# Kernel tuning notes

Measured on AMD Instinct MI355X. Metric: run time of the kernel, lower is better.

Reference implementation:

```python
import jax, jax.numpy as jnp
import numpy as np

OUT = 7          # output_size
SR = 2           # sampling_ratio
SCALES = (0.25, 0.125, 0.0625, 0.03125)
K_MIN, K_MAX = 2, 5   # -log2(scales[0]), -log2(scales[-1])
CANON_SCALE, CANON_LVL, EPS = 224.0, 4.0, 1e-6


def _roi_align_level(feat, b_idx, boxes, scale):
    """ROIAlign (maskrcnn-benchmark, non-aligned) of all boxes on one level.
    feat: [B,C,H,W], b_idx: [N] int, boxes: [N,4] xyxy in image coords.
    Returns [N,C,OUT,OUT]."""
    N = boxes.shape[0]
    H, W = feat.shape[2], feat.shape[3]
    x1 = boxes[:, 0] * scale
    y1 = boxes[:, 1] * scale
    x2 = boxes[:, 2] * scale
    y2 = boxes[:, 3] * scale
    roi_w = jnp.maximum(x2 - x1, 1.0)
    roi_h = jnp.maximum(y2 - y1, 1.0)
    bin_w = roi_w / OUT
    bin_h = roi_h / OUT
    # sample positions inside each bin, in bin units: [OUT*SR]
    sub = (jnp.arange(SR, dtype=feat.dtype) + 0.5) / SR
    grid1d = (jnp.arange(OUT, dtype=feat.dtype)[:, None] + sub[None, :]).reshape(-1)
    ys = y1[:, None] + bin_h[:, None] * grid1d[None, :]   # [N, OUT*SR]
    xs = x1[:, None] + bin_w[:, None] * grid1d[None, :]   # [N, OUT*SR]
    K = OUT * SR
    Yf = jnp.broadcast_to(ys[:, :, None], (N, K, K)).reshape(N, K * K)
    Xf = jnp.broadcast_to(xs[:, None, :], (N, K, K)).reshape(N, K * K)
    valid = (Yf >= -1.0) & (Yf <= H) & (Xf >= -1.0) & (Xf <= W)
    y = jnp.clip(Yf, 0.0, H - 1)
    x = jnp.clip(Xf, 0.0, W - 1)
    y0 = jnp.floor(y).astype(jnp.int32)
    x0 = jnp.floor(x).astype(jnp.int32)
    y1i = jnp.minimum(y0 + 1, H - 1)
    x1i = jnp.minimum(x0 + 1, W - 1)
    ly = y - y0
    lx = x - x0
    hy = 1.0 - ly
    hx = 1.0 - lx
    b = b_idx[:, None]  # [N,1] broadcasts with [N,K*K]
    def g(yi, xi):
        return feat[b, :, yi, xi]  # [N, K*K, C]
    val = (g(y0, x0) * (hy * hx)[..., None]
           + g(y0, x1i) * (hy * lx)[..., None]
           + g(y1i, x0) * (ly * hx)[..., None]
           + g(y1i, x1i) * (ly * lx)[..., None])
    val = jnp.where(valid[..., None], val, 0.0)
    # [N, OUT, SR, OUT, SR, C] -> average sampling points -> [N, OUT, OUT, C]
    val = val.reshape(N, OUT, SR, OUT, SR, -1).mean(axis=(2, 4))
    return jnp.transpose(val, (0, 3, 1, 2))  # [N, C, OUT, OUT]


def _map_levels(boxes):
    # BoxList.area with TO_REMOVE = 1 (xyxy mode)
    area = (boxes[:, 2] - boxes[:, 0] + 1.0) * (boxes[:, 3] - boxes[:, 1] + 1.0)
    s = jnp.sqrt(area)
    lvl = jnp.floor(CANON_LVL + jnp.log2(s / CANON_SCALE + EPS))
    lvl = jnp.clip(lvl, K_MIN, K_MAX)
    return lvl.astype(jnp.int32) - K_MIN  # 0..3


def setup_inputs() -> dict:
    key = jax.random.key(0)
    ks = jax.random.split(key, 10)
    N = 1024
    H_img, W_img = 800.0, 1216.0
    x1 = jax.random.uniform(ks[0], (N,), minval=0.0, maxval=W_img - 64.0)
    y1 = jax.random.uniform(ks[1], (N,), minval=0.0, maxval=H_img - 64.0)
    w = jax.random.uniform(ks[2], (N,), minval=8.0, maxval=500.0)
    h = jax.random.uniform(ks[3], (N,), minval=8.0, maxval=500.0)
    x2 = jnp.minimum(x1 + w, W_img - 1.0)
    y2 = jnp.minimum(y1 + h, H_img - 1.0)
    boxes = jnp.stack([x1, y1, x2, y2], axis=1).astype(jnp.float32)
    box_batch_idx = jnp.sort(jax.random.randint(ks[4], (N,), 0, 2)).astype(jnp.int32)
    f0 = jax.random.normal(ks[5], (2, 256, 200, 304), dtype=jnp.float32)
    f1 = jax.random.normal(ks[6], (2, 256, 100, 152), dtype=jnp.float32)
    f2 = jax.random.normal(ks[7], (2, 256, 50, 76), dtype=jnp.float32)
    f3 = jax.random.normal(ks[8], (2, 256, 25, 38), dtype=jnp.float32)
    return {"f0": f0, "f1": f1, "f2": f2, "f3": f3,
            "boxes": boxes, "box_batch_idx": box_batch_idx}


def reference(f0, f1, f2, f3, boxes, box_batch_idx):
    feats = (f0, f1, f2, f3)
    levels = _map_levels(boxes)  # [N] in 0..3
    out = None
    for lvl, (feat, scale) in enumerate(zip(feats, SCALES)):
        pooled = _roi_align_level(feat, box_batch_idx, boxes, scale)
        mask = (levels == lvl)[:, None, None, None]
        part = jnp.where(mask, pooled, 0.0)
        out = part if out is None else out + part
    return out  # [N, C, OUT, OUT]
```

## Files before the change

kernel.cpp:

```cpp
#include <hip/hip_runtime.h>
#include <math.h>

#define TILE_F 1792
#define B448   448
#define B896   896
#define NCH    8
#define MAXI   7
#define MAXIP  4
#define MAXI4  2
#define MAXK3  6

typedef __attribute__((address_space(3))) void lds_void;
typedef const __attribute__((address_space(1))) void g_void;

__device__ __forceinline__ void dma16(const float* g, float* l) {
  __builtin_amdgcn_global_load_lds((g_void*)g, (lds_void*)l, 16, 0, 0);
}
__device__ __forceinline__ void dma4(const float* g, float* l) {
  __builtin_amdgcn_global_load_lds((g_void*)g, (lds_void*)l, 4, 0, 0);
}
__device__ __forceinline__ void wait_vmcnt(int k) {
  switch (k) {
    case 0:  asm volatile("s_waitcnt vmcnt(0)"  ::: "memory"); break;
    case 1:  asm volatile("s_waitcnt vmcnt(1)"  ::: "memory"); break;
    case 2:  asm volatile("s_waitcnt vmcnt(2)"  ::: "memory"); break;
    case 3:  asm volatile("s_waitcnt vmcnt(3)"  ::: "memory"); break;
    case 4:  asm volatile("s_waitcnt vmcnt(4)"  ::: "memory"); break;
    case 5:  asm volatile("s_waitcnt vmcnt(5)"  ::: "memory"); break;
    case 6:  asm volatile("s_waitcnt vmcnt(6)"  ::: "memory"); break;
    case 7:  asm volatile("s_waitcnt vmcnt(7)"  ::: "memory"); break;
    case 8:  asm volatile("s_waitcnt vmcnt(8)"  ::: "memory"); break;
    case 9:  asm volatile("s_waitcnt vmcnt(9)"  ::: "memory"); break;
    case 10: asm volatile("s_waitcnt vmcnt(10)" ::: "memory"); break;
    case 11: asm volatile("s_waitcnt vmcnt(11)" ::: "memory"); break;
    case 12: asm volatile("s_waitcnt vmcnt(12)" ::: "memory"); break;
    case 13: asm volatile("s_waitcnt vmcnt(13)" ::: "memory"); break;
    case 14: asm volatile("s_waitcnt vmcnt(14)" ::: "memory"); break;
    case 15: asm volatile("s_waitcnt vmcnt(15)" ::: "memory"); break;
    case 16: asm volatile("s_waitcnt vmcnt(16)" ::: "memory"); break;
    case 17: asm volatile("s_waitcnt vmcnt(17)" ::: "memory"); break;
    default: asm volatile("s_waitcnt vmcnt(18)" ::: "memory"); break;
  }
}

#define COMPUTE_STORE(TP, CC)                                                  \
  if (lane < 49) {                                                             \
    float acc = 0.0f;                                                          \
    _Pragma("unroll")                                                          \
    for (int sy = 0; sy < 2; ++sy) {                                           \
      _Pragma("unroll")                                                        \
      for (int sx = 0; sx < 2; ++sx) {                                         \
        const float w00 = (TP)[rT[sy] + Cc0[sx]];                              \
        const float w01 = (TP)[rT[sy] + Cc1[sx]];                              \
        const float w10 = (TP)[rB[sy] + Cc0[sx]];                              \
        const float w11 = (TP)[rB[sy] + Cc1[sx]];                              \
        const float bil = HY[sy] * (HX[sx] * w00 + LX[sx] * w01)               \
                        + LY[sy] * (HX[sx] * w10 + LX[sx] * w11);              \
        acc += (VY[sy] * VX[sx]) * bil;                                        \
      }                                                                        \
    }                                                                          \
    outp[(CC) * 49] = acc * 0.25f;                                             \
  }

__global__ __launch_bounds__(128) void pooler_kernel(
    const float* __restrict__ f0, const float* __restrict__ f1,
    const float* __restrict__ f2, const float* __restrict__ f3,
    const float* __restrict__ boxes, const int* __restrict__ bidx,
    float* __restrict__ out, int N)
{
  __shared__ __align__(16) float tile[2][TILE_F];
  const int tid  = threadIdx.x;
  const int wave = tid >> 6, lane = tid & 63;
  const int n    = blockIdx.y;
  if (n >= N) return;

  const float bx1 = boxes[4*n+0], by1 = boxes[4*n+1];
  const float bx2 = boxes[4*n+2], by2 = boxes[4*n+3];
  const float area = (bx2 - bx1 + 1.0f) * (by2 - by1 + 1.0f);
  const float s    = sqrtf(area);
  int lvl = (int)floorf(4.0f + log2f(s / 224.0f + 1e-6f));
  lvl = lvl < 2 ? 2 : (lvl > 5 ? 5 : lvl);
  const int li = lvl - 2;

  int H, W; const float* feat; float scale;
  switch (li) {
    case 0:  feat = f0; H = 200; W = 304; scale = 0.25f;    break;
    case 1:  feat = f1; H = 100; W = 152; scale = 0.125f;   break;
    case 2:  feat = f2; H = 50;  W = 76;  scale = 0.0625f;  break;
    default: feat = f3; H = 25;  W = 38;  scale = 0.03125f; break;
  }
  const int b = bidx[n];
  const float x1s = bx1 * scale, y1s = by1 * scale;
  const float roiw = fmaxf(bx2 * scale - x1s, 1.0f);
  const float roih = fmaxf(by2 * scale - y1s, 1.0f);
  const float binw = roiw / 7.0f, binh = roih / 7.0f;
  const float Hm1f = (float)(H - 1), Wm1f = (float)(W - 1);
  const int   Hm1  = H - 1,          Wm1  = W - 1;

  const float yA = fminf(fmaxf(y1s + binh * 0.25f, 0.0f), Hm1f);
  const float yB = fminf(fmaxf(y1s + binh * 6.75f, 0.0f), Hm1f);
  const float xA = fminf(fmaxf(x1s + binw * 0.25f, 0.0f), Wm1f);
  const float xB = fminf(fmaxf(x1s + binw * 6.75f, 0.0f), Wm1f);
  const int y_lo  = (int)yA;
  const int y_hi  = min((int)yB + 1, Hm1);
  const int regH  = y_hi - y_lo + 1;
  const int x_lo4 = ((int)xA) & ~3;
  const int x_hi  = min((int)xB + 1, Wm1);
  const int row4  = ((x_hi - x_lo4 + 4) >> 2);
  const int regW4 = row4 << 2;

  const int bin = (lane < 49) ? lane : 0;
  const int ph = bin / 7, pw = bin - (bin / 7) * 7;
  int   rT[2], rB[2], Cc0[2], Cc1[2];
  float HY[2], LY[2], VY[2], HX[2], LX[2], VX[2];
#pragma unroll
  for (int t = 0; t < 2; ++t) {
    {
      const float g  = (float)ph + 0.25f + 0.5f * (float)t;
      const float Yf = y1s + binh * g;
      VY[t] = (Yf >= -1.0f && Yf <= (float)H) ? 1.0f : 0.0f;
      const float y = fminf(fmaxf(Yf, 0.0f), Hm1f);
      const int  y0 = (int)y;
      LY[t] = y - (float)y0;  HY[t] = 1.0f - LY[t];
      rT[t] = (y0 - y_lo) * regW4;
      rB[t] = (min(y0 + 1, Hm1) - y_lo) * regW4;
    }
    {
      const float g  = (float)pw + 0.25f + 0.5f * (float)t;
      const float Xf = x1s + binw * g;
      VX[t] = (Xf >= -1.0f && Xf <= (float)W) ? 1.0f : 0.0f;
      const float x = fminf(fmaxf(Xf, 0.0f), Wm1f);
      const int  x0 = (int)x;
      LX[t] = x - (float)x0;  HX[t] = 1.0f - LX[t];
      Cc0[t] = x0 - x_lo4;
      Cc1[t] = min(x0 + 1, Wm1) - x_lo4;
    }
  }

  const size_t planeHW = (size_t)H * W;
  const int    cbase   = (blockIdx.x << 4) + (wave << 3);
  const float* plane0  = feat + ((size_t)(b * 256 + cbase)) * planeHW
                              + (size_t)y_lo * W;
  float*       outp    = out + ((size_t)n * 256 + cbase) * 49 + lane;
  float*       myt     = tile[wave];

  if (li != 3) {
    int cnt4 = regH * row4;
    if (cnt4 > TILE_F / 4) cnt4 = TILE_F / 4;

    if (cnt4 <= B448 / 4) {
      int soff[MAXI4];
#pragma unroll
      for (int i = 0; i < MAXI4; ++i) {
        const int u = lane + (i << 6);
        if (u < cnt4) {
          const int r = u / row4;
          const int c = u - r * row4;
          soff[i] = r * W + x_lo4 + (c << 2);
        } else soff[i] = -1;
      }
      const int K = (cnt4 + 63) >> 6;

#pragma unroll
      for (int p = 0; p < 3; ++p) {
        const float* pl = plane0 + (size_t)p * planeHW;
        float* bf = myt + p * B448;
#pragma unroll
        for (int i = 0; i < MAXI4; ++i)
          if (soff[i] >= 0) dma16(pl + soff[i], bf + (i << 8));
      }

      for (int cc = 0; cc < NCH; ++cc) {
        asm volatile("s_waitcnt lgkmcnt(0)" ::: "memory");
        if (cc + 3 < NCH) {
          const float* pl = plane0 + (size_t)(cc + 3) * planeHW;
          float* bf = myt + ((cc + 3) & 3) * B448;
#pragma unroll
          for (int i = 0; i < MAXI4; ++i)
            if (soff[i] >= 0) dma16(pl + soff[i], bf + (i << 8));
        }
        const int rem = NCH - 1 - cc;
        wait_vmcnt(K * (rem > 3 ? 3 : rem));
        const float* bufC = myt + (cc & 3) * B448;
        COMPUTE_STORE(bufC, cc)
      }
    } else if (cnt4 <= B896 / 4) {
      int soff[MAXIP];
#pragma unroll
      for (int i = 0; i < MAXIP; ++i) {
        const int u = lane + (i << 6);
        if (u < cnt4) {
          const int r = u / row4;
          const int c = u - r * row4;
          soff[i] = r * W + x_lo4 + (c << 2);
        } else soff[i] = -1;
      }
      const int K = (cnt4 + 63) >> 6;

#pragma unroll
      for (int i = 0; i < MAXIP; ++i)
        if (soff[i] >= 0) dma16(plane0 + soff[i], myt + (i << 8));

      for (int cc = 0; cc < NCH; ++cc) {
        asm volatile("s_waitcnt lgkmcnt(0)" ::: "memory");
        if (cc + 1 < NCH) {
          const float* pl = plane0 + (size_t)(cc + 1) * planeHW;
          float* bf = myt + ((cc + 1) & 1) * B896;
#pragma unroll
          for (int i = 0; i < MAXIP; ++i)
            if (soff[i] >= 0) dma16(pl + soff[i], bf + (i << 8));
          wait_vmcnt(K);
        } else {
          asm volatile("s_waitcnt vmcnt(0)" ::: "memory");
        }
        const float* bufC = myt + (cc & 1) * B896;
        COMPUTE_STORE(bufC, cc)
      }
    } else {
      int soff[MAXI];
#pragma unroll
      for (int i = 0; i < MAXI; ++i) {
        const int u = lane + (i << 6);
        if (u < cnt4) {
          const int r = u / row4;
          const int c = u - r * row4;
          soff[i] = r * W + x_lo4 + (c << 2);
        } else soff[i] = -1;
      }
      for (int cc = 0; cc < NCH; ++cc) {
        const float* plane = plane0 + (size_t)cc * planeHW;
        asm volatile("s_waitcnt lgkmcnt(0)" ::: "memory");
#pragma unroll
        for (int i = 0; i < MAXI; ++i)
          if (soff[i] >= 0) dma16(plane + soff[i], myt + (i << 8));
        asm volatile("s_waitcnt vmcnt(0)" ::: "memory");
        COMPUTE_STORE(myt, cc)
      }
    }
  } else {
    int cntS = regH * regW4;
    if (cntS > (MAXK3 << 6)) cntS = MAXK3 << 6;
    int soff3[MAXK3];
#pragma unroll
    for (int k = 0; k < MAXK3; ++k) {
      const int u = (k << 6) + lane;
      if (u < cntS) {
        const int r   = u / regW4;
        const int c   = u - r * regW4;
        const int col = x_lo4 + c;
        soff3[k] = (col <= Wm1) ? (r * W + col) : -1;
      } else soff3[k] = -1;
    }
    const int K3 = (cntS + 63) >> 6;

#pragma unroll
    for (int p = 0; p < 3; ++p) {
      const float* pl = plane0 + (size_t)p * planeHW;
      float* bf = myt + p * B448;
#pragma unroll
      for (int k = 0; k < MAXK3; ++k)
        if (soff3[k] >= 0) dma4(pl + soff3[k], bf + (k << 6));
    }

    for (int cc = 0; cc < NCH; ++cc) {
      asm volatile("s_waitcnt lgkmcnt(0)" ::: "memory");
      if (cc + 3 < NCH) {
        const float* pl = plane0 + (size_t)(cc + 3) * planeHW;
        float* bf = myt + ((cc + 3) & 3) * B448;
#pragma unroll
        for (int k = 0; k < MAXK3; ++k)
          if (soff3[k] >= 0) dma4(pl + soff3[k], bf + (k << 6));
      }
      const int rem = NCH - 1 - cc;
      wait_vmcnt(K3 * (rem > 3 ? 3 : rem));
      const float* bufC = myt + (cc & 3) * B448;
      COMPUTE_STORE(bufC, cc)
    }
  }
}

extern "C" void kernel_launch(void* const* d_in, const int* in_sizes, int n_in,
                              void* d_out, int out_size, void* d_ws, size_t ws_size,
                              hipStream_t stream) {
  const float* f0    = (const float*)d_in[0];
  const float* f1    = (const float*)d_in[1];
  const float* f2    = (const float*)d_in[2];
  const float* f3    = (const float*)d_in[3];
  const float* boxes = (const float*)d_in[4];
  const int*   bidx  = (const int*)d_in[5];
  const int N = in_sizes[5];
  dim3 grid(16, N);
  pooler_kernel<<<grid, 128, 0, stream>>>(f0, f1, f2, f3, boxes, bidx,
                                          (float*)d_out, N);
}
```

Measured before the change: 279.0 us.

## Enlarge per-wave LDS and issue all channel DMAs up front for small regions

Per-wave LDS grows from 1792 to 4096 floats so small regions prefetch all 8 channel planes at once, and the stage-and-wait loops are replaced by a single issue phase followed by graded vmcnt waits. The largest-region path gains double buffering instead of a fully serial load-then-compute loop. Integer division for row/col offsets becomes a reciprocal multiply-shift. The vmcnt accounting now counts the interleaved output stores, and the larger LDS footprint may reduce occupancy.

```diff
diff --git a/kernel.cpp b/kernel.cpp
--- a/kernel.cpp
+++ b/kernel.cpp
@@ -1,13 +1,11 @@
 #include <hip/hip_runtime.h>
 #include <math.h>
 
-#define TILE_F 1792
-#define B448   448
-#define B896   896
-#define NCH    8
-#define MAXI   7
-#define MAXIP  4
-#define MAXI4  2
+#define WAVE_F 4096
+#define BPF    512
+#define MAXB   2
+#define MAXC4  4
+#define MAXD   8
 #define MAXK3  6
 
 typedef __attribute__((address_space(3))) void lds_void;
@@ -19,27 +17,15 @@
 __device__ __forceinline__ void dma4(const float* g, float* l) {
   __builtin_amdgcn_global_load_lds((g_void*)g, (lds_void*)l, 4, 0, 0);
 }
+#define WC(N) case N: asm volatile("s_waitcnt vmcnt(" #N ")" ::: "memory"); break;
 __device__ __forceinline__ void wait_vmcnt(int k) {
   switch (k) {
-    case 0:  asm volatile("s_waitcnt vmcnt(0)"  ::: "memory"); break;
-    case 1:  asm volatile("s_waitcnt vmcnt(1)"  ::: "memory"); break;
-    case 2:  asm volatile("s_waitcnt vmcnt(2)"  ::: "memory"); break;
-    case 3:  asm volatile("s_waitcnt vmcnt(3)"  ::: "memory"); break;
-    case 4:  asm volatile("s_waitcnt vmcnt(4)"  ::: "memory"); break;
-    case 5:  asm volatile("s_waitcnt vmcnt(5)"  ::: "memory"); break;
-    case 6:  asm volatile("s_waitcnt vmcnt(6)"  ::: "memory"); break;
-    case 7:  asm volatile("s_waitcnt vmcnt(7)"  ::: "memory"); break;
-    case 8:  asm volatile("s_waitcnt vmcnt(8)"  ::: "memory"); break;
-    case 9:  asm volatile("s_waitcnt vmcnt(9)"  ::: "memory"); break;
-    case 10: asm volatile("s_waitcnt vmcnt(10)" ::: "memory"); break;
-    case 11: asm volatile("s_waitcnt vmcnt(11)" ::: "memory"); break;
-    case 12: asm volatile("s_waitcnt vmcnt(12)" ::: "memory"); break;
-    case 13: asm volatile("s_waitcnt vmcnt(13)" ::: "memory"); break;
-    case 14: asm volatile("s_waitcnt vmcnt(14)" ::: "memory"); break;
-    case 15: asm volatile("s_waitcnt vmcnt(15)" ::: "memory"); break;
-    case 16: asm volatile("s_waitcnt vmcnt(16)" ::: "memory"); break;
-    case 17: asm volatile("s_waitcnt vmcnt(17)" ::: "memory"); break;
-    default: asm volatile("s_waitcnt vmcnt(18)" ::: "memory"); break;
+    WC(0) WC(1) WC(2) WC(3) WC(4) WC(5) WC(6) WC(7) WC(8) WC(9)
+    WC(10) WC(11) WC(12) WC(13) WC(14) WC(15) WC(16) WC(17) WC(18) WC(19)
+    WC(20) WC(21) WC(22) WC(23) WC(24) WC(25) WC(26) WC(27) WC(28) WC(29)
+    WC(30) WC(31) WC(32) WC(33) WC(34) WC(35) WC(36) WC(37) WC(38) WC(39)
+    WC(40) WC(41) WC(42) WC(43) WC(44) WC(45) WC(46) WC(47)
+    default: asm volatile("s_waitcnt vmcnt(48)" ::: "memory"); break;
   }
 }
 
@@ -68,7 +54,7 @@
     const float* __restrict__ boxes, const int* __restrict__ bidx,
     float* __restrict__ out, int N)
 {
-  __shared__ __align__(16) float tile[2][TILE_F];
+  __shared__ __align__(16) float tile[2][WAVE_F];
   const int tid  = threadIdx.x;
   const int wave = tid >> 6, lane = tid & 63;
   const int n    = blockIdx.y;
@@ -146,106 +132,108 @@
 
   if (li != 3) {
     int cnt4 = regH * row4;
-    if (cnt4 > TILE_F / 4) cnt4 = TILE_F / 4;
-
-    if (cnt4 <= B448 / 4) {
-      int soff[MAXI4];
-#pragma unroll
-      for (int i = 0; i < MAXI4; ++i) {
+    if (cnt4 > 512) cnt4 = 512;
+
+    const int Mrow = (int)(65536.0f / (float)row4) + 1;
+    const int K = (cnt4 + 63) >> 6;
+
+    if (cnt4 <= 128) {
+      int soff[MAXB];
+#pragma unroll
+      for (int i = 0; i < MAXB; ++i) {
         const int u = lane + (i << 6);
         if (u < cnt4) {
-          const int r = u / row4;
+          const int r = (u * Mrow) >> 16;
           const int c = u - r * row4;
           soff[i] = r * W + x_lo4 + (c << 2);
         } else soff[i] = -1;
       }
-      const int K = (cnt4 + 63) >> 6;
-
-#pragma unroll
-      for (int p = 0; p < 3; ++p) {
+#pragma unroll
+      for (int p = 0; p < 8; ++p) {
         const float* pl = plane0 + (size_t)p * planeHW;
-        float* bf = myt + p * B448;
-#pragma unroll
-        for (int i = 0; i < MAXI4; ++i)
+        float* bf = myt + p * BPF;
+#pragma unroll
+        for (int i = 0; i < MAXB; ++i)
           if (soff[i] >= 0) dma16(pl + soff[i], bf + (i << 8));
       }
-
-      for (int cc = 0; cc < NCH; ++cc) {
-        asm volatile("s_waitcnt lgkmcnt(0)" ::: "memory");
-        if (cc + 3 < NCH) {
-          const float* pl = plane0 + (size_t)(cc + 3) * planeHW;
-          float* bf = myt + ((cc + 3) & 3) * B448;
-#pragma unroll
-          for (int i = 0; i < MAXI4; ++i)
-            if (soff[i] >= 0) dma16(pl + soff[i], bf + (i << 8));
-        }
-        const int rem = NCH - 1 - cc;
-        wait_vmcnt(K * (rem > 3 ? 3 : rem));
-        const float* bufC = myt + (cc & 3) * B448;
+#pragma unroll
+      for (int cc = 0; cc < 8; ++cc) {
+        wait_vmcnt((7 - cc) * K + cc);
+        const float* bufC = myt + cc * BPF;
         COMPUTE_STORE(bufC, cc)
       }
-    } else if (cnt4 <= B896 / 4) {
-      int soff[MAXIP];
-#pragma unroll
-      for (int i = 0; i < MAXIP; ++i) {
+    } else if (cnt4 <= 256) {
+      int soff[MAXC4];
+#pragma unroll
+      for (int i = 0; i < MAXC4; ++i) {
         const int u = lane + (i << 6);
         if (u < cnt4) {
-          const int r = u / row4;
+          const int r = (u * Mrow) >> 16;
           const int c = u - r * row4;
           soff[i] = r * W + x_lo4 + (c << 2);
         } else soff[i] = -1;
       }
-      const int K = (cnt4 + 63) >> 6;
-
-#pragma unroll
-      for (int i = 0; i < MAXIP; ++i)
-        if (soff[i] >= 0) dma16(plane0 + soff[i], myt + (i << 8));
-
-      for (int cc = 0; cc < NCH; ++cc) {
+#pragma unroll
+      for (int p = 0; p < 3; ++p) {
+        const float* pl = plane0 + (size_t)p * planeHW;
+        float* bf = myt + ((p & 3) << 10);
+#pragma unroll
+        for (int i = 0; i < MAXC4; ++i)
+          if (soff[i] >= 0) dma16(pl + soff[i], bf + (i << 8));
+      }
+      for (int cc = 0; cc < 8; ++cc) {
         asm volatile("s_waitcnt lgkmcnt(0)" ::: "memory");
-        if (cc + 1 < NCH) {
-          const float* pl = plane0 + (size_t)(cc + 1) * planeHW;
-          float* bf = myt + ((cc + 1) & 1) * B896;
-#pragma unroll
-          for (int i = 0; i < MAXIP; ++i)
+        if (cc + 3 < 8) {
+          const float* pl = plane0 + (size_t)(cc + 3) * planeHW;
+          float* bf = myt + (((cc + 3) & 3) << 10);
+#pragma unroll
+          for (int i = 0; i < MAXC4; ++i)
             if (soff[i] >= 0) dma16(pl + soff[i], bf + (i << 8));
-          wait_vmcnt(K);
-        } else {
-          asm volatile("s_waitcnt vmcnt(0)" ::: "memory");
         }
-        const float* bufC = myt + (cc & 1) * B896;
+        const int nd = 7 - cc; 
+        wait_vmcnt((nd > 3 ? 3 : nd) * K + (cc > 3 ? 3 : cc));
+        const float* bufC = myt + ((cc & 3) << 10);
         COMPUTE_STORE(bufC, cc)
       }
     } else {
-      int soff[MAXI];
-#pragma unroll
-      for (int i = 0; i < MAXI; ++i) {
+      int soff[MAXD];
+#pragma unroll
+      for (int i = 0; i < MAXD; ++i) {
         const int u = lane + (i << 6);
         if (u < cnt4) {
-          const int r = u / row4;
+          const int r = (u * Mrow) >> 16;
           const int c = u - r * row4;
           soff[i] = r * W + x_lo4 + (c << 2);
         } else soff[i] = -1;
       }
-      for (int cc = 0; cc < NCH; ++cc) {
-        const float* plane = plane0 + (size_t)cc * planeHW;
+#pragma unroll
+      for (int i = 0; i < MAXD; ++i)
+        if (soff[i] >= 0) dma16(plane0 + soff[i], myt + (i << 8));
+
+      for (int cc = 0; cc < 8; ++cc) {
         asm volatile("s_waitcnt lgkmcnt(0)" ::: "memory");
-#pragma unroll
-        for (int i = 0; i < MAXI; ++i)
-          if (soff[i] >= 0) dma16(plane + soff[i], myt + (i << 8));
-        asm volatile("s_waitcnt vmcnt(0)" ::: "memory");
-        COMPUTE_STORE(myt, cc)
+        if (cc + 1 < 8) {
+          const float* pl = plane0 + (size_t)(cc + 1) * planeHW;
+          float* bf = myt + (((cc + 1) & 1) << 11);
+#pragma unroll
+          for (int i = 0; i < MAXD; ++i)
+            if (soff[i] >= 0) dma16(pl + soff[i], bf + (i << 8));
+        }
+        wait_vmcnt((cc < 7 ? K : 0) + (cc > 0 ? 1 : 0));
+        const float* bufC = myt + ((cc & 1) << 11);
+        COMPUTE_STORE(bufC, cc)
       }
     }
   } else {
     int cntS = regH * regW4;
     if (cntS > (MAXK3 << 6)) cntS = MAXK3 << 6;
+    const int MregW = (int)(65536.0f / (float)regW4) + 1;
     int soff3[MAXK3];
 #pragma unroll
     for (int k = 0; k < MAXK3; ++k) {
       const int u = (k << 6) + lane;
       if (u < cntS) {
-        const int r   = u / regW4;
+        const int r   = (u * MregW) >> 16;
         const int c   = u - r * regW4;
         const int col = x_lo4 + c;
         soff3[k] = (col <= Wm1) ? (r * W + col) : -1;
@@ -254,26 +242,17 @@
     const int K3 = (cntS + 63) >> 6;
 
 #pragma unroll
-    for (int p = 0; p < 3; ++p) {
+    for (int p = 0; p < 8; ++p) {
       const float* pl = plane0 + (size_t)p * planeHW;
-      float* bf = myt + p * B448;
+      float* bf = myt + p * BPF;
 #pragma unroll
       for (int k = 0; k < MAXK3; ++k)
         if (soff3[k] >= 0) dma4(pl + soff3[k], bf + (k << 6));
     }
-
-    for (int cc = 0; cc < NCH; ++cc) {
-      asm volatile("s_waitcnt lgkmcnt(0)" ::: "memory");
-      if (cc + 3 < NCH) {
-        const float* pl = plane0 + (size_t)(cc + 3) * planeHW;
-        float* bf = myt + ((cc + 3) & 3) * B448;
-#pragma unroll
-        for (int k = 0; k < MAXK3; ++k)
-          if (soff3[k] >= 0) dma4(pl + soff3[k], bf + (k << 6));
-      }
-      const int rem = NCH - 1 - cc;
-      wait_vmcnt(K3 * (rem > 3 ? 3 : rem));
-      const float* bufC = myt + (cc & 3) * B448;
+#pragma unroll
+    for (int cc = 0; cc < 8; ++cc) {
+      wait_vmcnt((7 - cc) * K3 + cc);
+      const float* bufC = myt + cc * BPF;
       COMPUTE_STORE(bufC, cc)
     }
   }
```

Measured after the change: 279.8 us. Within noise of the previous version (+0.3%).
